# Performance work log

Measured on AMD Instinct MI355X. Metric: run time of the kernel, lower is better.

## Reference

```python
import jax, jax.numpy as jnp
import numpy as np

N_NODES = 50000
N_EDGES = 800000
F_IN = 32
H = 128
N_REL = 4
MAX_DEG = 10
N_GRAPHS = 64
N_BLOCKS = 2


def setup_inputs() -> dict:
    key = jax.random.key(0)
    ks = jax.random.split(key, 20)
    s = 0.05
    return {
        "x": jax.random.normal(ks[0], (N_NODES, F_IN), jnp.float32),
        "edge_index": jax.random.randint(ks[1], (2, N_EDGES), 0, N_NODES, dtype=jnp.int32),
        "edge_attr": jax.random.randint(ks[2], (N_EDGES,), 0, N_REL, dtype=jnp.int32),
        "batch_idx": jnp.sort(jax.random.randint(ks[3], (N_NODES,), 0, N_GRAPHS, dtype=jnp.int32)),
        "embed_W": jax.random.normal(ks[4], (F_IN, H), jnp.float32) * s,
        "embed_b": jax.random.normal(ks[5], (H,), jnp.float32) * s,
        "rgcn_Wrel": jax.random.normal(ks[6], (N_BLOCKS, N_REL, H, H), jnp.float32) * s,
        "rgcn_Wroot": jax.random.normal(ks[7], (N_BLOCKS, H, H), jnp.float32) * s,
        "rgcn_b": jax.random.normal(ks[8], (N_BLOCKS, H), jnp.float32) * s,
        "mf_Wl": jax.random.normal(ks[9], (N_BLOCKS, MAX_DEG + 1, H, H), jnp.float32) * s,
        "mf_bl": jax.random.normal(ks[10], (N_BLOCKS, MAX_DEG + 1, H), jnp.float32) * s,
        "mf_Wr": jax.random.normal(ks[11], (N_BLOCKS, MAX_DEG + 1, H, H), jnp.float32) * s,
        "lin1_W": jax.random.normal(ks[12], (H, H), jnp.float32) * s,
        "lin1_b": jax.random.normal(ks[13], (H,), jnp.float32) * s,
        "lin2_W": jax.random.normal(ks[14], (H, 1), jnp.float32) * s,
        "lin2_b": jax.random.normal(ks[15], (1,), jnp.float32) * s,
    }


def _rgcn(x, src, dst, rel, Wrel, Wroot, b):
    # PyG RGCNConv with default aggr='mean': per-relation mean over incoming
    # edges, then per-relation weight, plus root transform and bias.
    seg = dst * N_REL + rel  # composite segment id: (node, relation)
    agg = jax.ops.segment_sum(x[src], seg, num_segments=N_NODES * N_REL)
    cnt = jax.ops.segment_sum(jnp.ones((seg.shape[0],), x.dtype), seg,
                              num_segments=N_NODES * N_REL)
    agg = (agg / jnp.maximum(cnt, 1.0)[:, None]).reshape(N_NODES, N_REL, H)
    return jnp.einsum('nrh,rho->no', agg, Wrel) + x @ Wroot + b


def _mfconv(x, src, dst, Wl, bl, Wr):
    # PyG MFConv: sum-aggregate neighbors, then per-degree-bucket linear heads
    # (degree = in-degree clamped to MAX_DEG); lin_r applied to root x (no bias).
    h = jax.ops.segment_sum(x[src], dst, num_segments=N_NODES)  # [N,H]
    deg = jax.ops.segment_sum(jnp.ones((src.shape[0],), jnp.int32), dst,
                              num_segments=N_NODES)
    deg = jnp.minimum(deg, MAX_DEG)  # [N]
    # out_all: [D+1, N, H] candidate outputs, one per degree bucket
    out_all = (jnp.einsum('nh,dho->dno', h, Wl)
               + jnp.einsum('nh,dho->dno', x, Wr)
               + bl[:, None, :])
    return jnp.take_along_axis(out_all, deg[None, :, None], axis=0)[0]


def reference(x, edge_index, edge_attr, batch_idx, embed_W, embed_b,
              rgcn_Wrel, rgcn_Wroot, rgcn_b, mf_Wl, mf_bl, mf_Wr,
              lin1_W, lin1_b, lin2_W, lin2_b):
    src, dst = edge_index[0], edge_index[1]
    h = x @ embed_W + embed_b
    for blk in range(N_BLOCKS):
        if blk > 0:  # first block uses Identity instead of ReLU
            h = jax.nn.relu(h)
        h = _rgcn(h, src, dst, edge_attr, rgcn_Wrel[blk], rgcn_Wroot[blk], rgcn_b[blk])
        h = jax.nn.relu(h)
        h = _mfconv(h, src, dst, mf_Wl[blk], mf_bl[blk], mf_Wr[blk])
    g = jax.ops.segment_sum(h, batch_idx, num_segments=N_GRAPHS)  # global_add_pool
    g = jax.nn.relu(g @ lin1_W + lin1_b)
    return g @ lin2_W + lin2_b
```

## Files before the change

### kernel.cpp

```cpp
#include <hip/hip_runtime.h>
#include <hip/hip_bf16.h>

#define NRELS 4
#define MAXDEG 10
#define NBUCK 11
#define POOL_CHUNKS 8

typedef __attribute__((ext_vector_type(8))) short s16x8;
typedef __attribute__((ext_vector_type(4))) float f32x4;
typedef __attribute__((ext_vector_type(8))) unsigned short u16x8;

__device__ inline unsigned short f2b(float f) {
  __hip_bfloat16 h = __float2bfloat16(f);
  return *reinterpret_cast<unsigned short*>(&h);
}
__device__ inline float b2f(unsigned short u) {
  union { unsigned int i; float f; } v;
  v.i = ((unsigned int)u) << 16;
  return v.f;
}
__device__ inline float blo(unsigned int v) {
  union { unsigned int i; float f; } x;
  x.i = v << 16;
  return x.f;
}
__device__ inline float bhi(unsigned int v) {
  union { unsigned int i; float f; } x;
  x.i = v & 0xffff0000u;
  return x.f;
}

typedef __attribute__((address_space(3))) unsigned int lds_uint;
typedef __attribute__((address_space(1))) const unsigned int glob_uint;
__device__ __forceinline__ void gld_lds16(const void* g, void* l) {
  __builtin_amdgcn_global_load_lds((glob_uint*)g, (lds_uint*)l, 16, 0, 0);
}


__global__ __launch_bounds__(512) void coarse_count(const int* __restrict__ dst,
                                                    int* __restrict__ bhist, int E) {
  __shared__ int lh[512];
  int t = threadIdx.x;
  lh[t] = 0;
  __syncthreads();
  int base = blockIdx.x * 4096;
  int lim = E - base;
  if (lim > 4096) lim = 4096;
  for (int i = t; i < lim; i += 512) atomicAdd(&lh[dst[base + i] >> 7], 1);
  __syncthreads();
  if (lh[t]) atomicAdd(&bhist[t], lh[t]);
}

__global__ __launch_bounds__(512) void coarse_scan(const int* __restrict__ bhist,
                                                   int* __restrict__ boff,
                                                   int* __restrict__ bcur, int NB, int E) {
  __shared__ int sd[512];
  int t = threadIdx.x;
  int v = (t < NB) ? bhist[t] : 0;
  sd[t] = v;
  __syncthreads();
  for (int o = 1; o < 512; o <<= 1) {
    int x = (t >= o) ? sd[t - o] : 0;
    __syncthreads();
    sd[t] += x;
    __syncthreads();
  }
  if (t < NB) {
    int st = sd[t] - v;
    boff[t] = st;
    bcur[t] = st;
  }
  if (t == 0) boff[NB] = E;
}

__global__ __launch_bounds__(512) void coarse_scatter(
    const int* __restrict__ src, const int* __restrict__ dst, const int* __restrict__ rel,
    int* __restrict__ bcur, uint2* __restrict__ ebuf, int E) {
  __shared__ int lhist[512];
  __shared__ int lstart[512];
  __shared__ int lcur[512];
  __shared__ int gbase[512];
  __shared__ uint2 stage[4096];
  int t = threadIdx.x;
  lhist[t] = 0;
  __syncthreads();
  int base = blockIdx.x * 4096;
  int lim = E - base;
  if (lim > 4096) lim = 4096;
  for (int i = t; i < lim; i += 512) atomicAdd(&lhist[dst[base + i] >> 7], 1);
  __syncthreads();
  int myc = lhist[t];
  lstart[t] = myc;
  __syncthreads();
  for (int o = 1; o < 512; o <<= 1) {
    int x = (t >= o) ? lstart[t - o] : 0;
    __syncthreads();
    lstart[t] += x;
    __syncthreads();
  }
  int incl = lstart[t];
  __syncthreads();
  lstart[t] = incl - myc;
  lcur[t] = 0;
  if (myc > 0) gbase[t] = atomicAdd(&bcur[t], myc);
  __syncthreads();
  for (int i = t; i < lim; i += 512) {
    int e = base + i;
    int d = dst[e];
    int b = d >> 7;
    int slot = lstart[b] + atomicAdd(&lcur[b], 1);
    stage[slot] = make_uint2((unsigned)(d * 4 + rel[e]), (unsigned)src[e]);
  }
  __syncthreads();
  for (int i = t; i < lim; i += 512) {
    uint2 val = stage[i];
    int b = (int)(val.x >> 9);
    ebuf[gbase[b] + (i - lstart[b])] = val;
  }
}

__global__ __launch_bounds__(512) void fine_count(const uint2* __restrict__ ebuf,
                                                  const int* __restrict__ boff,
                                                  int* __restrict__ cnt, int NSEG) {
  __shared__ int lh[512];
  int t = threadIdx.x;
  int b = blockIdx.x;
  lh[t] = 0;
  __syncthreads();
  int s = boff[b], e = boff[b + 1];
  for (int i = s + t; i < e; i += 512) atomicAdd(&lh[ebuf[i].x & 511], 1);
  __syncthreads();
  int gseg = b * 512 + t;
  if (gseg < NSEG) cnt[gseg] = lh[t];
}

__global__ __launch_bounds__(512) void place_local(const uint2* __restrict__ ebuf,
                                                   const int* __restrict__ boff,
                                                   const int* __restrict__ seg_start,
                                                   int* __restrict__ csr, int NSEG) {
  __shared__ int lcur[512];
  int t = threadIdx.x;
  int b = blockIdx.x;
  int gseg = b * 512 + t;
  lcur[t] = (gseg < NSEG) ? seg_start[gseg] : 0;
  __syncthreads();
  int s = boff[b], e = boff[b + 1];
  for (int i = s + t; i < e; i += 512) {
    uint2 v = ebuf[i];
    int pos = atomicAdd(&lcur[v.x & 511], 1);
    csr[pos] = (int)v.y;
  }
}

__global__ void prep_nodes(const int* __restrict__ cnt, float* __restrict__ inv,
                           int* __restrict__ deg, int* __restrict__ bucket,
                           int* __restrict__ hist, int N) {
  int n = blockIdx.x * 256 + threadIdx.x;
  int b = -1;
  if (n < N) {
    int d = 0;
    for (int r = 0; r < 4; r++) {
      int c = cnt[n * 4 + r];
      d += c;
      inv[n * 4 + r] = 1.0f / (float)(c > 1 ? c : 1);
    }
    deg[n] = d;
    b = d < MAXDEG ? d : MAXDEG;
    bucket[n] = b;
  }
  int lane = threadIdx.x & 63;
  for (int bb = 0; bb < NBUCK; bb++) {
    unsigned long long m = __ballot(b == bb);
    if (m == 0ULL) continue;
    int leader = __ffsll(m) - 1;
    if (lane == leader) atomicAdd(&hist[bb], __popcll(m));
  }
}

__global__ void calc_offsets(const int* __restrict__ hist, int* __restrict__ off,
                             int* __restrict__ fill) {
  if (threadIdx.x == 0) {
    int acc = 0;
    for (int b = 0; b < NBUCK; b++) {
      off[b] = acc;
      fill[b] = acc;
      acc += ((hist[b] + 63) >> 6) << 6;
    }
    off[NBUCK] = acc;
  }
}

__global__ void build_perm(const int* __restrict__ bucket, int* __restrict__ fill,
                           int* __restrict__ perm, int N) {
  int n = blockIdx.x * 256 + threadIdx.x;
  int b = (n < N) ? bucket[n] : -1;
  int lane = threadIdx.x & 63;
  for (int bb = 0; bb < NBUCK; bb++) {
    unsigned long long m = __ballot(b == bb);
    if (m == 0ULL) continue;
    int leader = __ffsll(m) - 1;
    int base = 0;
    if (lane == leader) base = atomicAdd(&fill[bb], __popcll(m));
    base = __shfl(base, leader);
    if (b == bb) {
      int idx = __popcll(m & ((1ULL << lane) - 1ULL));
      perm[base + idx] = n;
    }
  }
}

__global__ void assign_segments(const int* __restrict__ cnt, int* __restrict__ seg_start,
                                int* __restrict__ cursor, int NSEG) {
  __shared__ int sd[256];
  __shared__ int sbase;
  int t = threadIdx.x;
  int s = blockIdx.x * 256 + t;
  int v = (s < NSEG) ? cnt[s] : 0;
  sd[t] = v;
  __syncthreads();
  for (int o = 1; o < 256; o <<= 1) {
    int x = (t >= o) ? sd[t - o] : 0;
    __syncthreads();
    sd[t] += x;
    __syncthreads();
  }
  if (t == 255) sbase = atomicAdd(cursor, sd[255]);
  __syncthreads();
  if (s < NSEG) seg_start[s] = sbase + sd[t] - v;
}

__global__ void conv_rgcn_w(const float* __restrict__ Wrel, const float* __restrict__ Wroot,
                            unsigned short* __restrict__ Bt) {
  int t = blockIdx.x * 256 + threadIdx.x;
  if (t >= 2 * 128 * 640) return;
  int blk = t / 81920;
  int rem = t % 81920;
  int n = rem / 640;
  int k = rem % 640;
  float v;
  if (k < 512)
    v = Wrel[(size_t)blk * 65536 + (size_t)k * 128 + n];
  else
    v = Wroot[(size_t)blk * 16384 + (size_t)(k - 512) * 128 + n];
  Bt[t] = f2b(v);
}

__global__ void conv_mf_w(const float* __restrict__ Wl, const float* __restrict__ Wr,
                          unsigned short* __restrict__ Btm) {
  int t = blockIdx.x * 256 + threadIdx.x;
  if (t >= 2 * 11 * 128 * 256) return;
  int k = t & 255;
  int n = (t >> 8) & 127;
  int bb = (t >> 15) % 11;
  int blk = t / (11 * 128 * 256);
  float v;
  if (k < 128)
    v = Wl[(((size_t)blk * 11 + bb) * 128 + k) * 128 + n];
  else
    v = Wr[(((size_t)blk * 11 + bb) * 128 + (k - 128)) * 128 + n];
  Btm[t] = f2b(v);
}

#define ACC8(v)                                   \
  do {                                            \
    a0 += blo((v).x); a1 += bhi((v).x);           \
    a2 += blo((v).y); a3 += bhi((v).y);           \
    a4 += blo((v).z); a5 += bhi((v).z);           \
    a6 += blo((v).w); a7 += bhi((v).w);           \
  } while (0)

__global__ __launch_bounds__(256) void rgcn_gather(
    const unsigned short* __restrict__ hb, const int* __restrict__ csr,
    const int* __restrict__ seg_start, const int* __restrict__ cnt,
    const float* __restrict__ inv, unsigned short* __restrict__ ahat, int N) {
  int n = blockIdx.x * 16 + (threadIdx.x >> 4);
  if (n >= N) return;
  int c8 = (threadIdx.x & 15) * 8;
#pragma unroll
  for (int r = 0; r < 4; r++) {
    int seg = n * 4 + r;
    int st = seg_start[seg], cn = cnt[seg];
    float w = inv[seg];
    float a0 = 0.f, a1 = 0.f, a2 = 0.f, a3 = 0.f, a4 = 0.f, a5 = 0.f, a6 = 0.f, a7 = 0.f;
    int i = 0;
    for (; i + 2 <= cn; i += 2) {
      int p0 = csr[st + i], p1 = csr[st + i + 1];
      uint4 v0 = *(const uint4*)(hb + (size_t)p0 * 128 + c8);
      uint4 v1 = *(const uint4*)(hb + (size_t)p1 * 128 + c8);
      ACC8(v0);
      ACC8(v1);
    }
    if (i < cn) {
      uint4 v0 = *(const uint4*)(hb + (size_t)csr[st + i] * 128 + c8);
      ACC8(v0);
    }
    uint4 o;
    o.x = (unsigned int)f2b(a0 * w) | ((unsigned int)f2b(a1 * w) << 16);
    o.y = (unsigned int)f2b(a2 * w) | ((unsigned int)f2b(a3 * w) << 16);
    o.z = (unsigned int)f2b(a4 * w) | ((unsigned int)f2b(a5 * w) << 16);
    o.w = (unsigned int)f2b(a6 * w) | ((unsigned int)f2b(a7 * w) << 16);
    *(uint4*)(ahat + (size_t)n * 640 + r * 128 + c8) = o;
  }
  *(uint4*)(ahat + (size_t)n * 640 + 512 + c8) = *(const uint4*)(hb + (size_t)n * 128 + c8);
}

__global__ __launch_bounds__(256) void mf_gather(
    const unsigned short* __restrict__ hb, const int* __restrict__ csr,
    const int* __restrict__ seg_start, const int* __restrict__ deg,
    const int* __restrict__ perm, unsigned short* __restrict__ amf, int total) {
  int i = blockIdx.x * 16 + (threadIdx.x >> 4);
  if (i >= total) return;
  int c8 = (threadIdx.x & 15) * 8;
  int n = perm[i];
  if (n < 0) {
    uint4 z = {0u, 0u, 0u, 0u};
    *(uint4*)(amf + (size_t)i * 256 + c8) = z;
    *(uint4*)(amf + (size_t)i * 256 + 128 + c8) = z;
    return;
  }
  int st = seg_start[n * 4], dg = deg[n];
  float a0 = 0.f, a1 = 0.f, a2 = 0.f, a3 = 0.f, a4 = 0.f, a5 = 0.f, a6 = 0.f, a7 = 0.f;
  int i2 = 0;
  for (; i2 + 2 <= dg; i2 += 2) {
    int p0 = csr[st + i2], p1 = csr[st + i2 + 1];
    uint4 v0 = *(const uint4*)(hb + (size_t)p0 * 128 + c8);
    uint4 v1 = *(const uint4*)(hb + (size_t)p1 * 128 + c8);
    ACC8(v0);
    ACC8(v1);
  }
  if (i2 < dg) {
    uint4 v0 = *(const uint4*)(hb + (size_t)csr[st + i2] * 128 + c8);
    ACC8(v0);
  }
  uint4 o;
  o.x = (unsigned int)f2b(a0) | ((unsigned int)f2b(a1) << 16);
  o.y = (unsigned int)f2b(a2) | ((unsigned int)f2b(a3) << 16);
  o.z = (unsigned int)f2b(a4) | ((unsigned int)f2b(a5) << 16);
  o.w = (unsigned int)f2b(a6) | ((unsigned int)f2b(a7) << 16);
  *(uint4*)(amf + (size_t)i * 256 + c8) = o;
  *(uint4*)(amf + (size_t)i * 256 + 128 + c8) = *(const uint4*)(hb + (size_t)n * 128 + c8);
}

__global__ __launch_bounds__(256) void rgcn_mfma(const unsigned short* __restrict__ A,
                                                 const unsigned short* __restrict__ Bt,
                                                 const float* __restrict__ bias,
                                                 unsigned short* __restrict__ out, int N) {
  __shared__ unsigned char As[8192];
  __shared__ unsigned char Bs[16384];
  int t = threadIdx.x;
  int lane = t & 63, wave = t >> 6;
  int row = lane & 15, quad = lane >> 4;
  int m0 = blockIdx.x * 64;
  int nh = wave * 32;
  f32x4 acc[2][4];
#pragma unroll
  for (int i = 0; i < 2; i++)
#pragma unroll
    for (int j = 0; j < 4; j++) acc[i][j] = (f32x4){0.f, 0.f, 0.f, 0.f};

  for (int kt = 0; kt < 10; kt++) {
    int kb2 = kt * 128;
#pragma unroll
    for (int s = 0; s < 2; s++) {
      int o = s * 4096 + t * 16;
      int r = o >> 7, c = ((o >> 4) & 7) ^ (r & 7);
      int gr = m0 + r;
      if (gr >= N) gr = N - 1;
      gld_lds16((const char*)A + (size_t)gr * 1280 + kb2 + c * 16, As + o);
    }
#pragma unroll
    for (int s = 0; s < 4; s++) {
      int o = s * 4096 + t * 16;
      int r = o >> 7, c = ((o >> 4) & 7) ^ (r & 7);
      gld_lds16((const char*)Bt + (size_t)r * 1280 + kb2 + c * 16, Bs + o);
    }
    __syncthreads();
#pragma unroll
    for (int ks = 0; ks < 2; ks++) {
      int cch = ks * 4 + quad;
      s16x8 af[4], bf[2];
#pragma unroll
      for (int mt = 0; mt < 4; mt++) {
        int R = mt * 16 + row;
        af[mt] = *(const s16x8*)(As + R * 128 + ((cch ^ (R & 7)) << 4));
      }
#pragma unroll
      for (int nt = 0; nt < 2; nt++) {
        int R = nh + nt * 16 + row;
        bf[nt] = *(const s16x8*)(Bs + R * 128 + ((cch ^ (R & 7)) << 4));
      }
#pragma unroll
      for (int nt = 0; nt < 2; nt++)
#pragma unroll
        for (int mt = 0; mt < 4; mt++)
          acc[nt][mt] = __builtin_amdgcn_mfma_f32_16x16x32_bf16(af[mt], bf[nt], acc[nt][mt], 0, 0, 0);
    }
    __syncthreads();
  }
#pragma unroll
  for (int nt = 0; nt < 2; nt++) {
    int n = nh + nt * 16 + row;
    float bv = bias[n];
#pragma unroll
    for (int mt = 0; mt < 4; mt++) {
#pragma unroll
      for (int r4 = 0; r4 < 4; r4++) {
        int m = m0 + mt * 16 + quad * 4 + r4;
        if (m < N) out[(size_t)m * 128 + n] = f2b(fmaxf(acc[nt][mt][r4] + bv, 0.f));
      }
    }
  }
}

__global__ __launch_bounds__(256) void mf_mfma(const unsigned short* __restrict__ A,
                                               const unsigned short* __restrict__ Bt,
                                               const float* __restrict__ bl,
                                               const int* __restrict__ perm,
                                               const int* __restrict__ off,
                                               unsigned short* __restrict__ out, int relu_out) {
  __shared__ unsigned char As[8192];
  __shared__ unsigned char Bs[16384];
  __shared__ int soff[12];
  __shared__ int nodes[64];
  int t = threadIdx.x;
  int m0 = blockIdx.x * 64;
  if (t < 12) soff[t] = off[t];
  if (t >= 64 && t < 128) nodes[t - 64] = perm[m0 + t - 64];
  __syncthreads();
  if (m0 >= soff[11]) return;
  int b = 0;
  while (b < 10 && m0 >= soff[b + 1]) b++;
  const unsigned short* Bb = Bt + (size_t)b * 128 * 256;
  const float* bb = bl + b * 128;
  int lane = t & 63, wave = t >> 6;
  int row = lane & 15, quad = lane >> 4;
  int nh = wave * 32;
  f32x4 acc[2][4];
#pragma unroll
  for (int i = 0; i < 2; i++)
#pragma unroll
    for (int j = 0; j < 4; j++) acc[i][j] = (f32x4){0.f, 0.f, 0.f, 0.f};

  for (int kt = 0; kt < 4; kt++) {
    int kb2 = kt * 128;
#pragma unroll
    for (int s = 0; s < 2; s++) {
      int o = s * 4096 + t * 16;
      int r = o >> 7, c = ((o >> 4) & 7) ^ (r & 7);
      gld_lds16((const char*)A + (size_t)(m0 + r) * 512 + kb2 + c * 16, As + o);
    }
#pragma unroll
    for (int s = 0; s < 4; s++) {
      int o = s * 4096 + t * 16;
      int r = o >> 7, c = ((o >> 4) & 7) ^ (r & 7);
      gld_lds16((const char*)Bb + (size_t)r * 512 + kb2 + c * 16, Bs + o);
    }
    __syncthreads();
#pragma unroll
    for (int ks = 0; ks < 2; ks++) {
      int cch = ks * 4 + quad;
      s16x8 af[4], bf[2];
#pragma unroll
      for (int mt = 0; mt < 4; mt++) {
        int R = mt * 16 + row;
        af[mt] = *(const s16x8*)(As + R * 128 + ((cch ^ (R & 7)) << 4));
      }
#pragma unroll
      for (int nt = 0; nt < 2; nt++) {
        int R = nh + nt * 16 + row;
        bf[nt] = *(const s16x8*)(Bs + R * 128 + ((cch ^ (R & 7)) << 4));
      }
#pragma unroll
      for (int nt = 0; nt < 2; nt++)
#pragma unroll
        for (int mt = 0; mt < 4; mt++)
          acc[nt][mt] = __builtin_amdgcn_mfma_f32_16x16x32_bf16(af[mt], bf[nt], acc[nt][mt], 0, 0, 0);
    }
    __syncthreads();
  }
#pragma unroll
  for (int nt = 0; nt < 2; nt++) {
    int n = nh + nt * 16 + row;
    float bv = bb[n];
#pragma unroll
    for (int mt = 0; mt < 4; mt++) {
#pragma unroll
      for (int r4 = 0; r4 < 4; r4++) {
        int nd = nodes[mt * 16 + quad * 4 + r4];
        if (nd >= 0) {
          float v = acc[nt][mt][r4] + bv;
          if (relu_out) v = fmaxf(v, 0.f);
          out[(size_t)nd * 128 + n] = f2b(v);
        }
      }
    }
  }
}

__global__ __launch_bounds__(256) void embed_gemm(const float* __restrict__ x,
                                                  const float* __restrict__ W,
                                                  const float* __restrict__ bias,
                                                  unsigned short* __restrict__ out, int N) {
  __shared__ float As[64][33];
  __shared__ float Ws[32][128];
  int tid = threadIdx.x;
  int row0 = blockIdx.x * 64;
  int tx = tid & 15, ty = tid >> 4;
  int tx8 = tx * 8, ty4 = ty * 4;
  float acc[4][8];
#pragma unroll
  for (int j = 0; j < 8; j++) {
    float bv = bias[tx8 + j];
#pragma unroll
    for (int i = 0; i < 4; i++) acc[i][j] = bv;
  }
#pragma unroll
  for (int l = 0; l < 8; l++) {
    int lin = tid + l * 256;
    int r = lin >> 5, kk = lin & 31;
    int n = row0 + r;
    As[r][kk] = (n < N) ? x[(size_t)n * 32 + kk] : 0.f;
  }
#pragma unroll
  for (int l = 0; l < 16; l++) {
    int lin = tid + l * 256;
    Ws[lin >> 7][lin & 127] = W[lin];
  }
  __syncthreads();
#pragma unroll
  for (int kk = 0; kk < 32; kk++) {
    float a[4];
#pragma unroll
    for (int i = 0; i < 4; i++) a[i] = As[ty4 + i][kk];
    float4 w0 = *(const float4*)&Ws[kk][tx8];
    float4 w1 = *(const float4*)&Ws[kk][tx8 + 4];
    float w[8] = {w0.x, w0.y, w0.z, w0.w, w1.x, w1.y, w1.z, w1.w};
#pragma unroll
    for (int i = 0; i < 4; i++)
#pragma unroll
      for (int j = 0; j < 8; j++) acc[i][j] += a[i] * w[j];
  }
#pragma unroll
  for (int i = 0; i < 4; i++) {
    int n = row0 + ty4 + i;
    if (n < N) {
      u16x8 o;
#pragma unroll
      for (int j = 0; j < 8; j++) o[j] = f2b(acc[i][j]);
      *(u16x8*)&out[(size_t)n * 128 + tx8] = o;
    }
  }
}

__global__ void find_starts(const int* __restrict__ batch, int* __restrict__ starts,
                            int N, int G) {
  int g = threadIdx.x;
  if (g > G) return;
  int lo = 0, hi = N;
  while (lo < hi) {
    int m = (lo + hi) >> 1;
    if (batch[m] < g) lo = m + 1; else hi = m;
  }
  starts[g] = lo;
}

__global__ void pool2(const unsigned short* __restrict__ h, const int* __restrict__ starts,
                      float* __restrict__ g, int G) {
  int gr = blockIdx.x / POOL_CHUNKS;
  int ck = blockIdx.x % POOL_CHUNKS;
  int c = threadIdx.x;
  int s = starts[gr], e = starts[gr + 1];
  int len = e - s;
  int a = s + (int)(((long long)len * ck) / POOL_CHUNKS);
  int b = s + (int)(((long long)len * (ck + 1)) / POOL_CHUNKS);
  float sum = 0.f;
  for (int n = a; n < b; n++) sum += b2f(h[(size_t)n * 128 + c]);
  if (b > a) atomicAdd(&g[gr * 128 + c], sum);
}

__global__ void head_kernel(const float* __restrict__ g, const float* __restrict__ W1,
                            const float* __restrict__ b1, const float* __restrict__ W2,
                            const float* __restrict__ b2, float* __restrict__ out) {
  int bg = blockIdx.x;
  int o = threadIdx.x;
  __shared__ float gs[128];
  __shared__ float red[128];
  gs[o] = g[bg * 128 + o];
  __syncthreads();
  float acc = b1[o];
  for (int k = 0; k < 128; k++) acc += gs[k] * W1[k * 128 + o];
  acc = fmaxf(acc, 0.f);
  red[o] = acc * W2[o];
  __syncthreads();
  for (int s = 64; s > 0; s >>= 1) {
    if (o < s) red[o] += red[o + s];
    __syncthreads();
  }
  if (o == 0) out[bg] = red[0] + b2[0];
}

extern "C" void kernel_launch(void* const* d_in, const int* in_sizes, int n_in,
                              void* d_out, int out_size, void* d_ws, size_t ws_size,
                              hipStream_t stream) {
  const float* x = (const float*)d_in[0];
  const int* ei = (const int*)d_in[1];
  const int* ea = (const int*)d_in[2];
  const int* batch = (const int*)d_in[3];
  const float* embW = (const float*)d_in[4];
  const float* embB = (const float*)d_in[5];
  const float* Wrel = (const float*)d_in[6];
  const float* Wroot = (const float*)d_in[7];
  const float* rb = (const float*)d_in[8];
  const float* Wl = (const float*)d_in[9];
  const float* bl = (const float*)d_in[10];
  const float* Wr = (const float*)d_in[11];
  const float* l1W = (const float*)d_in[12];
  const float* l1b = (const float*)d_in[13];
  const float* l2W = (const float*)d_in[14];
  const float* l2b = (const float*)d_in[15];
  float* out = (float*)d_out;

  int N = in_sizes[0] / 32;
  int E = in_sizes[2];
  int G = out_size;
  int NSEG = N * 4;
  int NB = (N + 127) >> 7;

  char* p = (char*)d_ws;
  auto alloc = [&](size_t bytes) {
    char* r = p;
    p += (bytes + 255) & ~(size_t)255;
    return r;
  };
  int permCap = ((N + 63) / 64 + NBUCK) * 64;
  unsigned short* h_bf = (unsigned short*)alloc((size_t)N * 128 * 2);
  unsigned short* h2_bf = (unsigned short*)alloc((size_t)N * 128 * 2);
  unsigned short* ahat = (unsigned short*)alloc((size_t)N * 640 * 2);
  unsigned short* amf = (unsigned short*)alloc((size_t)permCap * 256 * 2);
  unsigned short* Btr = (unsigned short*)alloc((size_t)2 * 128 * 640 * 2);
  unsigned short* Btm = (unsigned short*)alloc((size_t)2 * 11 * 128 * 256 * 2);
  float* inv = (float*)alloc((size_t)NSEG * 4);
  int* cnt = (int*)alloc((size_t)NSEG * 4);
  int* seg_start = (int*)alloc((size_t)NSEG * 4);
  int* csr = (int*)alloc((size_t)E * 4);
  uint2* ebuf = (uint2*)alloc((size_t)E * 8);
  int* deg = (int*)alloc((size_t)N * 4);
  int* bucket = (int*)alloc((size_t)N * 4);
  int* perm = (int*)alloc((size_t)permCap * 4);
  int* bhist = (int*)alloc(512 * 4);
  int* boff = (int*)alloc(516 * 4);
  int* bcur = (int*)alloc(512 * 4);
  int* hist = (int*)alloc(64);
  int* off = (int*)alloc(64);
  int* fill = (int*)alloc(64);
  int* cursor = (int*)alloc(64);
  int* starts = (int*)alloc((size_t)(G + 1) * 4);
  float* g = (float*)alloc((size_t)G * 128 * 4);

  hipMemsetAsync(bhist, 0, 512 * 4, stream);
  hipMemsetAsync(hist, 0, 64, stream);
  hipMemsetAsync(cursor, 0, 64, stream);
  hipMemsetAsync(g, 0, (size_t)G * 128 * 4, stream);
  hipMemsetAsync(perm, 0xFF, (size_t)permCap * 4, stream);

  const int* src = ei;
  const int* dst = ei + E;

  int sblocks = (E + 4095) / 4096;
  coarse_count<<<sblocks, 512, 0, stream>>>(dst, bhist, E);
  coarse_scan<<<1, 512, 0, stream>>>(bhist, boff, bcur, NB, E);
  coarse_scatter<<<sblocks, 512, 0, stream>>>(src, dst, ea, bcur, ebuf, E);
  fine_count<<<NB, 512, 0, stream>>>(ebuf, boff, cnt, NSEG);
  prep_nodes<<<(N + 255) / 256, 256, 0, stream>>>(cnt, inv, deg, bucket, hist, N);
  calc_offsets<<<1, 64, 0, stream>>>(hist, off, fill);
  build_perm<<<(N + 255) / 256, 256, 0, stream>>>(bucket, fill, perm, N);
  assign_segments<<<(NSEG + 255) / 256, 256, 0, stream>>>(cnt, seg_start, cursor, NSEG);
  place_local<<<NB, 512, 0, stream>>>(ebuf, boff, seg_start, csr, NSEG);
  find_starts<<<1, 128, 0, stream>>>(batch, starts, N, G);
  conv_rgcn_w<<<(2 * 128 * 640 + 255) / 256, 256, 0, stream>>>(Wrel, Wroot, Btr);
  conv_mf_w<<<(2 * 11 * 128 * 256 + 255) / 256, 256, 0, stream>>>(Wl, Wr, Btm);

  embed_gemm<<<(N + 63) / 64, 256, 0, stream>>>(x, embW, embB, h_bf, N);

  int nb = (N + 63) / 64;
  int mfblocks = permCap / 64;
  for (int blk = 0; blk < 2; blk++) {
    rgcn_gather<<<(N + 15) / 16, 256, 0, stream>>>(h_bf, csr, seg_start, cnt, inv, ahat, N);
    rgcn_mfma<<<nb, 256, 0, stream>>>(ahat, Btr + (size_t)blk * 81920, rb + blk * 128, h2_bf, N);
    mf_gather<<<(permCap + 15) / 16, 256, 0, stream>>>(h2_bf, csr, seg_start, deg, perm, amf,
                                                       permCap);
    mf_mfma<<<mfblocks, 256, 0, stream>>>(amf, Btm + (size_t)blk * 11 * 128 * 256,
                                          bl + (size_t)blk * 11 * 128, perm, off, h_bf,
                                          (blk == 0) ? 1 : 0);
  }
  pool2<<<G * POOL_CHUNKS, 128, 0, stream>>>(h_bf, starts, g, G);
  head_kernel<<<G, 128, 0, stream>>>(g, l1W, l1b, l2W, l2b, out);
}
```

Baseline: 488.2 us.

## Read root features directly in GEMMs instead of copying into gathered buffers

The gather kernels no longer copy each node's own feature row into the staging buffers (ahat shrinks from 640 to 512 columns, amf from 256 to 128). The RGCN and MF MFMA kernels now load the root part of the K dimension straight from h_bf and h2_bf, with MF indexing through the permutation. The point is to cut redundant global writes and reads. The change also unrolls the neighbor gather loops by four, merges the two weight-conversion kernels, and folds the graph-start binary search into the pool kernel to save launches. A risk is that padded MF rows no longer get zeroed and are now read through nodes[r]; the clamp to node 0 only affects rows that are discarded.

```diff
diff --git a/kernel.cpp b/kernel.cpp
--- a/kernel.cpp
+++ b/kernel.cpp
@@ -35,7 +35,6 @@
 __device__ __forceinline__ void gld_lds16(const void* g, void* l) {
   __builtin_amdgcn_global_load_lds((glob_uint*)g, (lds_uint*)l, 16, 0, 0);
 }
-
 
 __global__ __launch_bounds__(512) void coarse_count(const int* __restrict__ dst,
                                                     int* __restrict__ bhist, int E) {
@@ -229,36 +228,35 @@
   if (s < NSEG) seg_start[s] = sbase + sd[t] - v;
 }
 
-__global__ void conv_rgcn_w(const float* __restrict__ Wrel, const float* __restrict__ Wroot,
-                            unsigned short* __restrict__ Bt) {
+__global__ void conv_weights(const float* __restrict__ Wrel, const float* __restrict__ Wroot,
+                             const float* __restrict__ Wl, const float* __restrict__ Wr,
+                             unsigned short* __restrict__ Bt, unsigned short* __restrict__ Btm) {
   int t = blockIdx.x * 256 + threadIdx.x;
-  if (t >= 2 * 128 * 640) return;
-  int blk = t / 81920;
-  int rem = t % 81920;
-  int n = rem / 640;
-  int k = rem % 640;
-  float v;
-  if (k < 512)
-    v = Wrel[(size_t)blk * 65536 + (size_t)k * 128 + n];
-  else
-    v = Wroot[(size_t)blk * 16384 + (size_t)(k - 512) * 128 + n];
-  Bt[t] = f2b(v);
-}
-
-__global__ void conv_mf_w(const float* __restrict__ Wl, const float* __restrict__ Wr,
-                          unsigned short* __restrict__ Btm) {
-  int t = blockIdx.x * 256 + threadIdx.x;
-  if (t >= 2 * 11 * 128 * 256) return;
-  int k = t & 255;
-  int n = (t >> 8) & 127;
-  int bb = (t >> 15) % 11;
-  int blk = t / (11 * 128 * 256);
+  if (t < 2 * 128 * 640) {
+    int blk = t / 81920;
+    int rem = t % 81920;
+    int n = rem / 640;
+    int k = rem % 640;
+    float v;
+    if (k < 512)
+      v = Wrel[(size_t)blk * 65536 + (size_t)k * 128 + n];
+    else
+      v = Wroot[(size_t)blk * 16384 + (size_t)(k - 512) * 128 + n];
+    Bt[t] = f2b(v);
+    return;
+  }
+  int t2 = t - 2 * 128 * 640;
+  if (t2 >= 2 * 11 * 128 * 256) return;
+  int k = t2 & 255;
+  int n = (t2 >> 8) & 127;
+  int bb = (t2 >> 15) % 11;
+  int blk = t2 / (11 * 128 * 256);
   float v;
   if (k < 128)
     v = Wl[(((size_t)blk * 11 + bb) * 128 + k) * 128 + n];
   else
     v = Wr[(((size_t)blk * 11 + bb) * 128 + (k - 128)) * 128 + n];
-  Btm[t] = f2b(v);
+  Btm[t2] = f2b(v);
 }
 
 #define ACC8(v)                                   \
@@ -283,12 +281,25 @@
     float w = inv[seg];
     float a0 = 0.f, a1 = 0.f, a2 = 0.f, a3 = 0.f, a4 = 0.f, a5 = 0.f, a6 = 0.f, a7 = 0.f;
     int i = 0;
-    for (; i + 2 <= cn; i += 2) {
+    for (; i + 4 <= cn; i += 4) {
+      int p0 = csr[st + i], p1 = csr[st + i + 1];
+      int p2 = csr[st + i + 2], p3 = csr[st + i + 3];
+      uint4 v0 = *(const uint4*)(hb + (size_t)p0 * 128 + c8);
+      uint4 v1 = *(const uint4*)(hb + (size_t)p1 * 128 + c8);
+      uint4 v2 = *(const uint4*)(hb + (size_t)p2 * 128 + c8);
+      uint4 v3 = *(const uint4*)(hb + (size_t)p3 * 128 + c8);
+      ACC8(v0);
+      ACC8(v1);
+      ACC8(v2);
+      ACC8(v3);
+    }
+    if (i + 2 <= cn) {
       int p0 = csr[st + i], p1 = csr[st + i + 1];
       uint4 v0 = *(const uint4*)(hb + (size_t)p0 * 128 + c8);
       uint4 v1 = *(const uint4*)(hb + (size_t)p1 * 128 + c8);
       ACC8(v0);
       ACC8(v1);
+      i += 2;
     }
     if (i < cn) {
       uint4 v0 = *(const uint4*)(hb + (size_t)csr[st + i] * 128 + c8);
@@ -299,9 +310,8 @@
     o.y = (unsigned int)f2b(a2 * w) | ((unsigned int)f2b(a3 * w) << 16);
     o.z = (unsigned int)f2b(a4 * w) | ((unsigned int)f2b(a5 * w) << 16);
     o.w = (unsigned int)f2b(a6 * w) | ((unsigned int)f2b(a7 * w) << 16);
-    *(uint4*)(ahat + (size_t)n * 640 + r * 128 + c8) = o;
-  }
-  *(uint4*)(ahat + (size_t)n * 640 + 512 + c8) = *(const uint4*)(hb + (size_t)n * 128 + c8);
+    *(uint4*)(ahat + (size_t)n * 512 + r * 128 + c8) = o;
+  }
 }
 
 __global__ __launch_bounds__(256) void mf_gather(
@@ -312,21 +322,29 @@
   if (i >= total) return;
   int c8 = (threadIdx.x & 15) * 8;
   int n = perm[i];
-  if (n < 0) {
-    uint4 z = {0u, 0u, 0u, 0u};
-    *(uint4*)(amf + (size_t)i * 256 + c8) = z;
-    *(uint4*)(amf + (size_t)i * 256 + 128 + c8) = z;
-    return;
-  }
+  if (n < 0) return;
   int st = seg_start[n * 4], dg = deg[n];
   float a0 = 0.f, a1 = 0.f, a2 = 0.f, a3 = 0.f, a4 = 0.f, a5 = 0.f, a6 = 0.f, a7 = 0.f;
   int i2 = 0;
-  for (; i2 + 2 <= dg; i2 += 2) {
+  for (; i2 + 4 <= dg; i2 += 4) {
+    int p0 = csr[st + i2], p1 = csr[st + i2 + 1];
+    int p2 = csr[st + i2 + 2], p3 = csr[st + i2 + 3];
+    uint4 v0 = *(const uint4*)(hb + (size_t)p0 * 128 + c8);
+    uint4 v1 = *(const uint4*)(hb + (size_t)p1 * 128 + c8);
+    uint4 v2 = *(const uint4*)(hb + (size_t)p2 * 128 + c8);
+    uint4 v3 = *(const uint4*)(hb + (size_t)p3 * 128 + c8);
+    ACC8(v0);
+    ACC8(v1);
+    ACC8(v2);
+    ACC8(v3);
+  }
+  if (i2 + 2 <= dg) {
     int p0 = csr[st + i2], p1 = csr[st + i2 + 1];
     uint4 v0 = *(const uint4*)(hb + (size_t)p0 * 128 + c8);
     uint4 v1 = *(const uint4*)(hb + (size_t)p1 * 128 + c8);
     ACC8(v0);
     ACC8(v1);
+    i2 += 2;
   }
   if (i2 < dg) {
     uint4 v0 = *(const uint4*)(hb + (size_t)csr[st + i2] * 128 + c8);
@@ -337,11 +355,11 @@
   o.y = (unsigned int)f2b(a2) | ((unsigned int)f2b(a3) << 16);
   o.z = (unsigned int)f2b(a4) | ((unsigned int)f2b(a5) << 16);
   o.w = (unsigned int)f2b(a6) | ((unsigned int)f2b(a7) << 16);
-  *(uint4*)(amf + (size_t)i * 256 + c8) = o;
-  *(uint4*)(amf + (size_t)i * 256 + 128 + c8) = *(const uint4*)(hb + (size_t)n * 128 + c8);
+  *(uint4*)(amf + (size_t)i * 128 + c8) = o;
 }
 
 __global__ __launch_bounds__(256) void rgcn_mfma(const unsigned short* __restrict__ A,
+                                                 const unsigned short* __restrict__ hroot,
                                                  const unsigned short* __restrict__ Bt,
                                                  const float* __restrict__ bias,
                                                  unsigned short* __restrict__ out, int N) {
@@ -366,7 +384,9 @@
       int r = o >> 7, c = ((o >> 4) & 7) ^ (r & 7);
       int gr = m0 + r;
       if (gr >= N) gr = N - 1;
-      gld_lds16((const char*)A + (size_t)gr * 1280 + kb2 + c * 16, As + o);
+      const char* gsrc = (kt < 8) ? ((const char*)A + (size_t)gr * 1024 + kb2 + c * 16)
+                                  : ((const char*)hroot + (size_t)gr * 256 + (kb2 - 1024) + c * 16);
+      gld_lds16(gsrc, As + o);
     }
 #pragma unroll
     for (int s = 0; s < 4; s++) {
@@ -413,6 +433,7 @@
 }
 
 __global__ __launch_bounds__(256) void mf_mfma(const unsigned short* __restrict__ A,
+                                               const unsigned short* __restrict__ hroot,
                                                const unsigned short* __restrict__ Bt,
                                                const float* __restrict__ bl,
                                                const int* __restrict__ perm,
@@ -447,7 +468,15 @@
     for (int s = 0; s < 2; s++) {
       int o = s * 4096 + t * 16;
       int r = o >> 7, c = ((o >> 4) & 7) ^ (r & 7);
-      gld_lds16((const char*)A + (size_t)(m0 + r) * 512 + kb2 + c * 16, As + o);
+      const char* gsrc;
+      if (kt < 2) {
+        gsrc = (const char*)A + (size_t)(m0 + r) * 256 + kb2 + c * 16;
+      } else {
+        int nd = nodes[r];
+        if (nd < 0) nd = 0;
+        gsrc = (const char*)hroot + (size_t)nd * 256 + (kb2 - 512) + c * 16;
+      }
+      gld_lds16(gsrc, As + o);
     }
 #pragma unroll
     for (int s = 0; s < 4; s++) {
@@ -552,24 +581,23 @@
   }
 }
 
-__global__ void find_starts(const int* __restrict__ batch, int* __restrict__ starts,
-                            int N, int G) {
-  int g = threadIdx.x;
-  if (g > G) return;
+__global__ void pool2(const unsigned short* __restrict__ h, const int* __restrict__ batch,
+                      float* __restrict__ g, int N, int G) {
+  int gr = blockIdx.x / POOL_CHUNKS;
+  int ck = blockIdx.x % POOL_CHUNKS;
+  int c = threadIdx.x;
   int lo = 0, hi = N;
   while (lo < hi) {
     int m = (lo + hi) >> 1;
-    if (batch[m] < g) lo = m + 1; else hi = m;
-  }
-  starts[g] = lo;
-}
-
-__global__ void pool2(const unsigned short* __restrict__ h, const int* __restrict__ starts,
-                      float* __restrict__ g, int G) {
-  int gr = blockIdx.x / POOL_CHUNKS;
-  int ck = blockIdx.x % POOL_CHUNKS;
-  int c = threadIdx.x;
-  int s = starts[gr], e = starts[gr + 1];
+    if (batch[m] < gr) lo = m + 1; else hi = m;
+  }
+  int s = lo;
+  lo = s; hi = N;
+  while (lo < hi) {
+    int m = (lo + hi) >> 1;
+    if (batch[m] < gr + 1) lo = m + 1; else hi = m;
+  }
+  int e = lo;
   int len = e - s;
   int a = s + (int)(((long long)len * ck) / POOL_CHUNKS);
   int b = s + (int)(((long long)len * (ck + 1)) / POOL_CHUNKS);
@@ -635,8 +663,8 @@
   int permCap = ((N + 63) / 64 + NBUCK) * 64;
   unsigned short* h_bf = (unsigned short*)alloc((size_t)N * 128 * 2);
   unsigned short* h2_bf = (unsigned short*)alloc((size_t)N * 128 * 2);
-  unsigned short* ahat = (unsigned short*)alloc((size_t)N * 640 * 2);
-  unsigned short* amf = (unsigned short*)alloc((size_t)permCap * 256 * 2);
+  unsigned short* ahat = (unsigned short*)alloc((size_t)N * 512 * 2);
+  unsigned short* amf = (unsigned short*)alloc((size_t)permCap * 128 * 2);
   unsigned short* Btr = (unsigned short*)alloc((size_t)2 * 128 * 640 * 2);
   unsigned short* Btm = (unsigned short*)alloc((size_t)2 * 11 * 128 * 256 * 2);
   float* inv = (float*)alloc((size_t)NSEG * 4);
@@ -654,7 +682,6 @@
   int* off = (int*)alloc(64);
   int* fill = (int*)alloc(64);
   int* cursor = (int*)alloc(64);
-  int* starts = (int*)alloc((size_t)(G + 1) * 4);
   float* g = (float*)alloc((size_t)G * 128 * 4);
 
   hipMemsetAsync(bhist, 0, 512 * 4, stream);
@@ -676,9 +703,8 @@
   build_perm<<<(N + 255) / 256, 256, 0, stream>>>(bucket, fill, perm, N);
   assign_segments<<<(NSEG + 255) / 256, 256, 0, stream>>>(cnt, seg_start, cursor, NSEG);
   place_local<<<NB, 512, 0, stream>>>(ebuf, boff, seg_start, csr, NSEG);
-  find_starts<<<1, 128, 0, stream>>>(batch, starts, N, G);
-  conv_rgcn_w<<<(2 * 128 * 640 + 255) / 256, 256, 0, stream>>>(Wrel, Wroot, Btr);
-  conv_mf_w<<<(2 * 11 * 128 * 256 + 255) / 256, 256, 0, stream>>>(Wl, Wr, Btm);
+  int convTotal = 2 * 128 * 640 + 2 * 11 * 128 * 256;
+  conv_weights<<<(convTotal + 255) / 256, 256, 0, stream>>>(Wrel, Wroot, Wl, Wr, Btr, Btm);
 
   embed_gemm<<<(N + 63) / 64, 256, 0, stream>>>(x, embW, embB, h_bf, N);
 
@@ -686,13 +712,14 @@
   int mfblocks = permCap / 64;
   for (int blk = 0; blk < 2; blk++) {
     rgcn_gather<<<(N + 15) / 16, 256, 0, stream>>>(h_bf, csr, seg_start, cnt, inv, ahat, N);
-    rgcn_mfma<<<nb, 256, 0, stream>>>(ahat, Btr + (size_t)blk * 81920, rb + blk * 128, h2_bf, N);
+    rgcn_mfma<<<nb, 256, 0, stream>>>(ahat, h_bf, Btr + (size_t)blk * 81920, rb + blk * 128,
+                                      h2_bf, N);
     mf_gather<<<(permCap + 15) / 16, 256, 0, stream>>>(h2_bf, csr, seg_start, deg, perm, amf,
                                                        permCap);
-    mf_mfma<<<mfblocks, 256, 0, stream>>>(amf, Btm + (size_t)blk * 11 * 128 * 256,
+    mf_mfma<<<mfblocks, 256, 0, stream>>>(amf, h2_bf, Btm + (size_t)blk * 11 * 128 * 256,
                                           bl + (size_t)blk * 11 * 128, perm, off, h_bf,
                                           (blk == 0) ? 1 : 0);
   }
-  pool2<<<G * POOL_CHUNKS, 128, 0, stream>>>(h_bf, starts, g, G);
+  pool2<<<G * POOL_CHUNKS, 128, 0, stream>>>(h_bf, batch, g, N, G);
   head_kernel<<<G, 128, 0, stream>>>(g, l1W, l1b, l2W, l2b, out);
 }
```

New measurement: 467.8 us. 4.2% less time.
